# Performance work log

Measured on AMD Instinct MI355X. Metric: run time of the kernel, lower is better.

Reference implementation:

```python
import jax, jax.numpy as jnp
import numpy as np

ENC_DIMS = [768, 2048, 1024, 512, 128]   # [in_dim] + layers + [e_dim]
DEC_DIMS = ENC_DIMS[::-1]
NUM_LEVELS = 4    # len(num_emb_list)
NUM_EXPERTS = 10
CODEBOOK_K = 256  # codes per level per expert
BETA = 0.001


def setup_inputs() -> dict:
    key = jax.random.key(0)
    B = 32768
    ks = jax.random.split(key, 16)
    inp = {}
    inp["x"] = jax.random.normal(ks[0], (B, ENC_DIMS[0]), dtype=jnp.float32)
    inp["labels"] = jax.random.randint(ks[1], (B,), 0, NUM_EXPERTS)
    i = 2
    for l in range(4):
        inp[f"enc_w{l}"] = jax.random.normal(ks[i], (ENC_DIMS[l], ENC_DIMS[l + 1]), dtype=jnp.float32) * 0.02
        inp[f"enc_b{l}"] = jnp.zeros((ENC_DIMS[l + 1],), dtype=jnp.float32)
        i += 1
    for l in range(4):
        inp[f"dec_w{l}"] = jax.random.normal(ks[i], (DEC_DIMS[l], DEC_DIMS[l + 1]), dtype=jnp.float32) * 0.02
        inp[f"dec_b{l}"] = jnp.zeros((DEC_DIMS[l + 1],), dtype=jnp.float32)
        i += 1
    # per-level, per-expert codebooks: [L, E, K, D]
    inp["cb"] = jax.random.normal(ks[i], (NUM_LEVELS, NUM_EXPERTS, CODEBOOK_K, ENC_DIMS[-1]), dtype=jnp.float32) * 0.02
    return inp


def _mlp(h, ws, bs):
    # Linear + ReLU between layers, no activation on the last layer (dropout=0, bn=False)
    n = len(ws)
    for i in range(n):
        h = h @ ws[i] + bs[i]
        if i < n - 1:
            h = jax.nn.relu(h)
    return h


def _residual_quantize(z, labels, cb):
    # z: [B, D]; labels: [B] expert ids; cb: [L, E, K, D]
    res = z
    qsum = jnp.zeros_like(z)
    loss = jnp.zeros((), dtype=z.dtype)
    idx_list = []
    for l in range(cb.shape[0]):  # small fixed loop over quantization levels
        cbl = cb[l]  # [E, K, D]
        # squared distances to each sample's expert codebook:
        # d[b,k] = ||res_b||^2 - 2 res_b . C[lab_b,k] + ||C[lab_b,k]||^2
        dots = jnp.einsum('bd,ekd->bek', res, cbl)                       # [B, E, K]
        dots = jnp.take_along_axis(dots, labels[:, None, None], axis=1)[:, 0]  # [B, K]
        cnorm = jnp.sum(cbl * cbl, axis=-1)[labels]                      # [B, K]
        d = jnp.sum(res * res, axis=-1, keepdims=True) - 2.0 * dots + cnorm
        idx = jnp.argmin(d, axis=-1)                                     # [B]
        q = cbl[labels, idx]                                             # [B, D] gather
        # codebook loss + beta * commitment loss
        loss = loss + jnp.mean((q - jax.lax.stop_gradient(res)) ** 2) \
                    + BETA * jnp.mean((jax.lax.stop_gradient(q) - res) ** 2)
        qsum = qsum + q
        res = res - q
        idx_list.append(idx)
    # straight-through estimator on the full quantized vector
    x_q = z + jax.lax.stop_gradient(qsum - z)
    indices = jnp.stack(idx_list, axis=1)  # [B, L]
    return x_q, loss, indices


def reference(x, labels,
              enc_w0, enc_b0, enc_w1, enc_b1, enc_w2, enc_b2, enc_w3, enc_b3,
              dec_w0, dec_b0, dec_w1, dec_b1, dec_w2, dec_b2, dec_w3, dec_b3,
              cb):
    enc_ws = [enc_w0, enc_w1, enc_w2, enc_w3]
    enc_bs = [enc_b0, enc_b1, enc_b2, enc_b3]
    dec_ws = [dec_w0, dec_w1, dec_w2, dec_w3]
    dec_bs = [dec_b0, dec_b1, dec_b2, dec_b3]
    z = _mlp(x, enc_ws, enc_bs)                      # encoder -> [B, e_dim]
    x_q, rq_loss, indices = _residual_quantize(z, labels, cb)
    out = _mlp(x_q, dec_ws, dec_bs)                  # decoder -> [B, in_dim]
    return out, rq_loss, indices, x_q
```

## Files before the change

kernel.cpp:

```cpp
#include <hip/hip_runtime.h>
#include <cstdint>
#include <cstddef>


typedef _Float16 half8  __attribute__((ext_vector_type(8)));
typedef short    short8 __attribute__((ext_vector_type(8)));
typedef float    f32x4  __attribute__((ext_vector_type(4)));

__device__ __forceinline__ uint16_t f32_to_bf16(float v) {
    uint32_t u = __float_as_uint(v);
    u += 0x7fff + ((u >> 16) & 1);
    return (uint16_t)(u >> 16);
}
__device__ __forceinline__ uint16_t f32_to_f16_bits(float v) {
    _Float16 h = (_Float16)v;
    return __builtin_bit_cast(uint16_t, h);
}
__device__ __forceinline__ void split16(float v, uint16_t& hb, uint16_t& lb) {
    hb = f32_to_f16_bits(v);
    float hf = (float)__builtin_bit_cast(_Float16, hb);
    lb = f32_to_f16_bits((v - hf) * 2048.0f);
}

__device__ __forceinline__ float wave_sum(float v) {
    #pragma unroll
    for (int off = 32; off > 0; off >>= 1)
        v += __shfl_xor(v, off, 64);
    return v;
}

#define GLOAD_LDS16(g, l)                                                      \
    __builtin_amdgcn_global_load_lds(                                          \
        (const __attribute__((address_space(1))) void*)(g),                    \
        (__attribute__((address_space(3))) void*)(l), 16, 0, 0)

__device__ __forceinline__ void wait_vm(int nf) {
    if (nf >= 12)     asm volatile("s_waitcnt vmcnt(12)" ::: "memory");
    else if (nf >= 8) asm volatile("s_waitcnt vmcnt(8)"  ::: "memory");
    else if (nf >= 6) asm volatile("s_waitcnt vmcnt(6)"  ::: "memory");
    else if (nf >= 4) asm volatile("s_waitcnt vmcnt(4)"  ::: "memory");
    else              asm volatile("s_waitcnt vmcnt(0)"  ::: "memory");
}
__device__ __forceinline__ void wait_lg0() { asm volatile("s_waitcnt lgkmcnt(0)" ::: "memory"); }

template<bool F16> struct VecT        { using type = half8;  };
template<>         struct VecT<false> { using type = short8; };

__device__ __forceinline__ f32x4 mfma16(half8 a, half8 b, f32x4 c) {
    return __builtin_amdgcn_mfma_f32_16x16x32_f16(a, b, c, 0, 0, 0);
}
__device__ __forceinline__ f32x4 mfma16(short8 a, short8 b, f32x4 c) {
    return __builtin_amdgcn_mfma_f32_16x16x32_bf16(a, b, c, 0, 0, 0);
}

template<int NPL, int NBUF, int BN, bool ISF16, bool CORR, bool RELU, int OUT>
__global__ __launch_bounds__(256, 3)
void gemm_mfma(const uint16_t* __restrict__ A, const uint16_t* __restrict__ Wt,
               const float* __restrict__ bias,
               float* __restrict__ Cf, uint16_t* __restrict__ C0,
               uint16_t* __restrict__ C1, int M, int K, int N) {
    using vec8 = typename VecT<ISF16>::type;
    constexpr int APL    = 8192;
    constexpr int BPL    = BN * 64;
    constexpr int TILE_B = NPL * (APL + BPL);
    constexpr int BSHOT  = BN / 64;
    constexpr int NR     = BN / 32;
    constexpr int LPT    = NPL * (2 + BSHOT);
    __shared__ __align__(16) char lds[NBUF * TILE_B];

    const int t    = threadIdx.x;
    const int lane = t & 63, wave = t >> 6;
    const int wm = wave >> 1, wn = wave & 1;
    const int bm = blockIdx.y, bn = blockIdx.x;

    const size_t planeA = (size_t)M * K;
    const size_t planeB = (size_t)N * K;

    const int r0 = t >> 2,        c0 = (t & 3) ^ ((r0 >> 1) & 3);
    const int r1 = 64 + (t >> 2), c1 = (t & 3) ^ ((r1 >> 1) & 3);

    const uint16_t* gA0 = A + (size_t)(bm * 128 + r0) * K + c0 * 8;
    const uint16_t* gA1 = A + (size_t)(bm * 128 + r1) * K + c1 * 8;
    const uint16_t* gB[2];
    gB[0] = Wt + (size_t)(bn * BN + r0) * K + c0 * 8;
    if (BSHOT == 2) gB[1] = Wt + (size_t)(bn * BN + r1) * K + c1 * 8;

    const int wb = wave * 1024;
    const int l15 = lane & 15, quad = lane >> 4;
    const int cpf = quad ^ ((l15 >> 1) & 3);
    const int aoff = ((wm * 64 + l15) * 4 + cpf) * 16;
    const int boff = ((wn * (BN / 2) + l15) * 4 + cpf) * 16;

    f32x4 accM[4][NR], accC[4][NR];
    #pragma unroll
    for (int mi = 0; mi < 4; ++mi)
        #pragma unroll
        for (int nj = 0; nj < NR; ++nj)
            #pragma unroll
            for (int r = 0; r < 4; ++r) { accM[mi][nj][r] = 0.f; if (CORR) accC[mi][nj][r] = 0.f; }

    const int nt = K >> 5;

    auto stage = [&](int ti, int bi) {
        char* bA = (char*)lds + bi * TILE_B;
        char* bB = bA + NPL * APL;
        const int kb = ti * 32;
        #pragma unroll
        for (int p = 0; p < NPL; ++p) {
            GLOAD_LDS16(gA0 + (size_t)p * planeA + kb, bA + p * APL + wb);
            GLOAD_LDS16(gA1 + (size_t)p * planeA + kb, bA + p * APL + 4096 + wb);
            #pragma unroll
            for (int s = 0; s < BSHOT; ++s)
                GLOAD_LDS16(gB[s] + (size_t)p * planeB + kb, bB + p * BPL + s * 4096 + wb);
        }
    };

    #pragma unroll
    for (int i = 0; i < NBUF - 1; ++i) stage(i, i);

    int cur = 0;
    for (int it = 0; it < nt; ++it) {
        const int nx = it + NBUF - 1;
        if (nx < nt) {
            int bi = cur + NBUF - 1; if (bi >= NBUF) bi -= NBUF;
            stage(nx, bi);
        }
        const int rem = nt - 1 - it;
        const int nf  = (rem < NBUF - 1 ? rem : NBUF - 1) * LPT;
        wait_vm(nf);
        __builtin_amdgcn_sched_barrier(0);
        __builtin_amdgcn_s_barrier();
        __builtin_amdgcn_sched_barrier(0);

        char* bA = (char*)lds + cur * TILE_B;
        char* bB = bA + NPL * APL;

        vec8 a0[4], b0[NR];
        #pragma unroll
        for (int i = 0; i < 4; ++i)
            a0[i] = *(const vec8*)(bA + aoff + i * 1024);
        #pragma unroll
        for (int i = 0; i < NR; ++i)
            b0[i] = *(const vec8*)(bB + boff + i * 1024);
        #pragma unroll
        for (int mi = 0; mi < 4; ++mi)
            #pragma unroll
            for (int nj = 0; nj < NR; ++nj)
                accM[mi][nj] = mfma16(a0[mi], b0[nj], accM[mi][nj]);

        if (CORR) {
            vec8 b1[NR];
            #pragma unroll
            for (int i = 0; i < NR; ++i)
                b1[i] = *(const vec8*)(bB + BPL + boff + i * 1024);
            #pragma unroll
            for (int mi = 0; mi < 4; ++mi)
                #pragma unroll
                for (int nj = 0; nj < NR; ++nj)
                    accC[mi][nj] = mfma16(a0[mi], b1[nj], accC[mi][nj]);
            vec8 a1[4];
            #pragma unroll
            for (int i = 0; i < 4; ++i)
                a1[i] = *(const vec8*)(bA + APL + aoff + i * 1024);
            #pragma unroll
            for (int mi = 0; mi < 4; ++mi)
                #pragma unroll
                for (int nj = 0; nj < NR; ++nj)
                    accC[mi][nj] = mfma16(a1[mi], b0[nj], accC[mi][nj]);
        }

        wait_lg0();
        __builtin_amdgcn_sched_barrier(0);
        __builtin_amdgcn_s_barrier();
        __builtin_amdgcn_sched_barrier(0);

        cur = cur + 1; if (cur == NBUF) cur = 0;
    }

    if (CORR) {
        #pragma unroll
        for (int mi = 0; mi < 4; ++mi)
            #pragma unroll
            for (int nj = 0; nj < NR; ++nj)
                #pragma unroll
                for (int r = 0; r < 4; ++r)
                    accM[mi][nj][r] += accC[mi][nj][r] * (1.0f / 2048.0f);
    }

    const int colb = bn * BN + wn * (BN / 2) + l15;
    const int rowb = bm * 128 + wm * 64 + quad * 4;
    float bz[NR];
    #pragma unroll
    for (int nj = 0; nj < NR; ++nj) bz[nj] = bias[colb + nj * 16];

    #pragma unroll
    for (int mi = 0; mi < 4; ++mi)
        #pragma unroll
        for (int nj = 0; nj < NR; ++nj)
            #pragma unroll
            for (int r = 0; r < 4; ++r) {
                float v = accM[mi][nj][r] + bz[nj];
                if (RELU) v = fmaxf(v, 0.f);
                const size_t o = (size_t)(rowb + mi * 16 + r) * N + colb + nj * 16;
                if (OUT == 0) {
                    Cf[o] = v;
                } else if (OUT == 1) {
                    uint16_t hb, lb; split16(v, hb, lb);
                    C0[o] = hb; C1[o] = lb;
                } else {
                    C0[o] = f32_to_bf16(v);
                }
            }
}

template<int MODE>
__global__ __launch_bounds__(256)
void prep_w(const float* __restrict__ W, uint16_t* __restrict__ out, int K, int N) {
    __shared__ float tile[32][33];
    const int tx = threadIdx.x & 31, ty = threadIdx.x >> 5;
    const int n0 = blockIdx.x * 32, k0 = blockIdx.y * 32;
    #pragma unroll
    for (int i = 0; i < 4; ++i)
        tile[ty + i * 8][tx] = W[(size_t)(k0 + ty + i * 8) * N + n0 + tx];
    __syncthreads();
    #pragma unroll
    for (int i = 0; i < 4; ++i) {
        float v = tile[tx][ty + i * 8];
        size_t o = (size_t)(n0 + ty + i * 8) * K + k0 + tx;
        if (MODE == 0) {
            uint16_t hb, lb; split16(v, hb, lb);
            out[o] = hb;
            out[o + (size_t)N * K] = lb;
        } else {
            out[o] = f32_to_bf16(v);
        }
    }
}

__global__ __launch_bounds__(256)
void split_x(const float* __restrict__ x, uint16_t* __restrict__ hi,
             uint16_t* __restrict__ lo, int n4) {
    int i = blockIdx.x * 256 + threadIdx.x;
    const int stride = gridDim.x * 256;
    for (; i < n4; i += stride) {
        float4 v = ((const float4*)x)[i];
        ushort4 h, l;
        split16(v.x, h.x, l.x); split16(v.y, h.y, l.y);
        split16(v.z, h.z, l.z); split16(v.w, h.w, l.w);
        ((ushort4*)hi)[i] = h;
        ((ushort4*)lo)[i] = l;
    }
}

__global__ __launch_bounds__(256)
void prep_cb2(const float* __restrict__ cb, uint16_t* __restrict__ cbh,
              uint16_t* __restrict__ cbl, float* __restrict__ cnorm) {
    const int t = threadIdx.x, wave = t >> 6, lane = t & 63;
    const int row = blockIdx.x * 4 + wave;
    const float2 v = *(const float2*)(cb + (size_t)row * 128 + lane * 2);
    ushort2 h, l;
    split16(v.x, h.x, l.x); split16(v.y, h.y, l.y);
    *(ushort2*)(cbh + (size_t)row * 128 + lane * 2) = h;
    *(ushort2*)(cbl + (size_t)row * 128 + lane * 2) = l;
    const float s = wave_sum(v.x * v.x + v.y * v.y);
    if (lane == 0) cnorm[row] = s;
}

__global__ __launch_bounds__(256)
void hist_kernel(const int* __restrict__ labels, int* __restrict__ off,
                 int* __restrict__ cnt) {
    __shared__ int h[10];
    const int t = threadIdx.x;
    if (t < 10) h[t] = 0;
    __syncthreads();
    for (int i = t; i < 32768; i += 256) atomicAdd(&h[labels[i]], 1);
    __syncthreads();
    if (t == 0) {
        int a = 0;
        for (int e = 0; e < 10; ++e) { off[e] = a; a += h[e]; }
        off[10] = a;
    }
    if (t < 10) cnt[t] = 0;
}

__global__ __launch_bounds__(256)
void scatter_kernel(const int* __restrict__ labels, const int* __restrict__ off,
                    int* __restrict__ cnt, int* __restrict__ perm) {
    __shared__ int h[10], base[10];
    const int t = threadIdx.x;
    const int r = blockIdx.x * 256 + t;
    if (t < 10) h[t] = 0;
    __syncthreads();
    const int e = labels[r];
    const int lr = atomicAdd(&h[e], 1);
    __syncthreads();
    if (t < 10) base[t] = (h[t] > 0) ? atomicAdd(&cnt[t], h[t]) : 0;
    __syncthreads();
    perm[off[e] + base[e] + lr] = r;
}

__global__ __launch_bounds__(256)
void gather_kernel(const int* __restrict__ perm, const float* __restrict__ z,
                   float* __restrict__ resp, uint16_t* __restrict__ resph,
                   uint16_t* __restrict__ respl) {
    const int t = threadIdx.x, wave = t >> 6, lane = t & 63;
    const int p = blockIdx.x * 4 + wave;
    const int r = perm[p];
    const float2 v = *(const float2*)(z + (size_t)r * 128 + lane * 2);
    *(float2*)(resp + (size_t)p * 128 + lane * 2) = v;
    ushort2 h, l;
    split16(v.x, h.x, l.x); split16(v.y, h.y, l.y);
    *(ushort2*)(resph + (size_t)p * 128 + lane * 2) = h;
    *(ushort2*)(respl + (size_t)p * 128 + lane * 2) = l;
}

#define BETA_F 0.001f

template<bool LAST>
__global__ __launch_bounds__(256)
void rq_level(int l, const int* __restrict__ off, const int* __restrict__ perm,
              const float* __restrict__ cb, const uint16_t* __restrict__ cbh,
              const uint16_t* __restrict__ cbl, const float* __restrict__ cnorm,
              float* __restrict__ resp, uint16_t* __restrict__ resph,
              uint16_t* __restrict__ respl, const float* __restrict__ z,
              float* __restrict__ out_idx, float* __restrict__ out_xq,
              float* __restrict__ out_loss, uint16_t* __restrict__ xqbf) {
    __shared__ __align__(16) uint16_t Ah[2048], Al[2048];
    __shared__ __align__(16) uint16_t Bh[8192], Bl[8192];
    __shared__ float redv[64][4];
    __shared__ int   redk[64][4];
    __shared__ int   kwin[64];
    __shared__ float wl[4];
    __shared__ int   soff[11];

    const int t = threadIdx.x, lane = t & 63, wave = t >> 6;
    if (t < 11) soff[t] = off[t];
    __syncthreads();

    int e = -1, tile = 0, acc = 0;
    #pragma unroll
    for (int i = 0; i < 10; ++i) {
        const int nb = (soff[i + 1] - soff[i] + 63) >> 6;
        if ((int)blockIdx.x < acc + nb && e < 0) { e = i; tile = blockIdx.x - acc; }
        acc += nb;
    }
    if (e < 0) return;
    const int p0 = soff[e] + tile * 64;
    const int nrows = min(64, soff[e + 1] - p0);
    const int le = l * 10 + e;

    const int l15 = lane & 15, quad = lane >> 4;
    const int wn = wave;

    const int ar = t >> 2;
    const int ac = (t & 3) ^ ((ar >> 1) & 3);
    const int arp = p0 + ((ar < nrows) ? ar : 0);
    const uint16_t* gAh = resph + (size_t)arp * 128 + ac * 8;
    const uint16_t* gAl = respl + (size_t)arp * 128 + ac * 8;
    const uint16_t* cbh_b = cbh + (size_t)le * 256 * 128;
    const uint16_t* cbl_b = cbl + (size_t)le * 256 * 128;

    f32x4 accM[4][4], accC[4][4];
    #pragma unroll
    for (int mi = 0; mi < 4; ++mi)
        #pragma unroll
        for (int nj = 0; nj < 4; ++nj)
            #pragma unroll
            for (int r = 0; r < 4; ++r) { accM[mi][nj][r] = 0.f; accC[mi][nj][r] = 0.f; }

    const int cpf = quad ^ ((l15 >> 1) & 3);

    for (int kc = 0; kc < 4; ++kc) {
        const int kk = kc * 32;
        __syncthreads();
        GLOAD_LDS16(gAh + kk, (char*)Ah + t * 16);
        GLOAD_LDS16(gAl + kk, (char*)Al + t * 16);
        #pragma unroll
        for (int rnd = 0; rnd < 4; ++rnd) {
            const int j = rnd * 256 + t;
            const int br = j >> 2;
            const int bc = (j & 3) ^ ((br >> 1) & 3);
            GLOAD_LDS16(cbh_b + (size_t)br * 128 + kk + bc * 8, (char*)Bh + j * 16);
            GLOAD_LDS16(cbl_b + (size_t)br * 128 + kk + bc * 8, (char*)Bl + j * 16);
        }
        __syncthreads();

        half8 ah[4], bh[4];
        #pragma unroll
        for (int i = 0; i < 4; ++i) {
            ah[i] = *(const half8*)((char*)Ah + ((i * 16 + l15) * 4 + cpf) * 16);
            bh[i] = *(const half8*)((char*)Bh + ((wn * 64 + i * 16 + l15) * 4 + cpf) * 16);
        }
        #pragma unroll
        for (int mi = 0; mi < 4; ++mi)
            #pragma unroll
            for (int nj = 0; nj < 4; ++nj)
                accM[mi][nj] = mfma16(ah[mi], bh[nj], accM[mi][nj]);

        half8 bl4[4];
        #pragma unroll
        for (int i = 0; i < 4; ++i)
            bl4[i] = *(const half8*)((char*)Bl + ((wn * 64 + i * 16 + l15) * 4 + cpf) * 16);
        #pragma unroll
        for (int mi = 0; mi < 4; ++mi)
            #pragma unroll
            for (int nj = 0; nj < 4; ++nj)
                accC[mi][nj] = mfma16(ah[mi], bl4[nj], accC[mi][nj]);

        half8 al4[4];
        #pragma unroll
        for (int i = 0; i < 4; ++i)
            al4[i] = *(const half8*)((char*)Al + ((i * 16 + l15) * 4 + cpf) * 16);
        #pragma unroll
        for (int mi = 0; mi < 4; ++mi)
            #pragma unroll
            for (int nj = 0; nj < 4; ++nj)
                accC[mi][nj] = mfma16(al4[mi], bh[nj], accC[mi][nj]);
    }

    float cnv[4];
    #pragma unroll
    for (int nj = 0; nj < 4; ++nj)
        cnv[nj] = cnorm[le * 256 + wn * 64 + nj * 16 + l15];

    #pragma unroll
    for (int mi = 0; mi < 4; ++mi)
        #pragma unroll
        for (int r = 0; r < 4; ++r) {
            float bv = 1e30f; int bk = 0;
            #pragma unroll
            for (int nj = 0; nj < 4; ++nj) {
                const float d = cnv[nj] -
                    2.f * (accM[mi][nj][r] + accC[mi][nj][r] * (1.0f / 2048.0f));
                const int k = wn * 64 + nj * 16 + l15;
                if (d < bv || (d == bv && k < bk)) { bv = d; bk = k; }
            }
            #pragma unroll
            for (int o = 1; o < 16; o <<= 1) {
                const float ov = __shfl_xor(bv, o, 64);
                const int   ok = __shfl_xor(bk, o, 64);
                if (ov < bv || (ov == bv && ok < bk)) { bv = ov; bk = ok; }
            }
            const int row = mi * 16 + quad * 4 + r;
            if (l15 == 0) { redv[row][wn] = bv; redk[row][wn] = bk; }
        }
    __syncthreads();

    if (wave == 0) {
        const int row = lane;
        if (row < nrows) {
            float bv = redv[row][0]; int bk = redk[row][0];
            #pragma unroll
            for (int w = 1; w < 4; ++w) {
                const float ov = redv[row][w]; const int ok = redk[row][w];
                if (ov < bv || (ov == bv && ok < bk)) { bv = ov; bk = ok; }
            }
            kwin[row] = bk;
            out_idx[(size_t)perm[p0 + row] * 4 + l] = (float)bk;
        }
    }
    __syncthreads();

    float lossw = 0.f;
    for (int i = 0; i < 16; ++i) {
        const int row = wave * 16 + i;
        if (row < nrows) {
            const int p = p0 + row;
            const int k = kwin[row];
            const float2 q2 = *(const float2*)(cb + ((size_t)le * 256 + k) * 128 + lane * 2);
            float2 r2 = *(float2*)(resp + (size_t)p * 128 + lane * 2);
            const float n0 = r2.x - q2.x, n1 = r2.y - q2.y;
            *(float2*)(resp + (size_t)p * 128 + lane * 2) = make_float2(n0, n1);
            if (!LAST) {
                ushort2 h, lo;
                split16(n0, h.x, lo.x); split16(n1, h.y, lo.y);
                *(ushort2*)(resph + (size_t)p * 128 + lane * 2) = h;
                *(ushort2*)(respl + (size_t)p * 128 + lane * 2) = lo;
            }
            lossw += wave_sum(n0 * n0 + n1 * n1);
            if (LAST) {
                const int orig = perm[p];
                const float2 z2 = *(const float2*)(z + (size_t)orig * 128 + lane * 2);
                const float xq0 = z2.x - n0, xq1 = z2.y - n1;
                out_xq[(size_t)orig * 128 + lane * 2]     = xq0;
                out_xq[(size_t)orig * 128 + lane * 2 + 1] = xq1;
                ushort2 xb; xb.x = f32_to_bf16(xq0); xb.y = f32_to_bf16(xq1);
                *(ushort2*)(xqbf + (size_t)orig * 128 + lane * 2) = xb;
            }
        }
    }
    if (lane == 0) wl[wave] = lossw;
    __syncthreads();
    if (t == 0)
        atomicAdd(out_loss, (wl[0] + wl[1] + wl[2] + wl[3]) *
                            ((1.0f + BETA_F) / (32768.0f * 128.0f)));
}


extern "C" void kernel_launch(void* const* d_in, const int* in_sizes, int n_in,
                              void* d_out, int out_size, void* d_ws, size_t ws_size,
                              hipStream_t stream) {
    const float* x      = (const float*)d_in[0];
    const int*   labels = (const int*)d_in[1];
    const float* ew[4]  = {(const float*)d_in[2], (const float*)d_in[4],
                           (const float*)d_in[6], (const float*)d_in[8]};
    const float* eb[4]  = {(const float*)d_in[3], (const float*)d_in[5],
                           (const float*)d_in[7], (const float*)d_in[9]};
    const float* dw[4]  = {(const float*)d_in[10], (const float*)d_in[12],
                           (const float*)d_in[14], (const float*)d_in[16]};
    const float* db[4]  = {(const float*)d_in[11], (const float*)d_in[13],
                           (const float*)d_in[15], (const float*)d_in[17]};
    const float* cb     = (const float*)d_in[18];

    float* out = (float*)d_out;
    const size_t LOSS_OFF = 25165824;
    const size_t IDX_OFF  = 25165825;
    const size_t XQ_OFF   = 25296897;

    char* W = (char*)d_ws;
    size_t off_b = 0;
    auto alloc = [&](size_t bytes) { char* p = W + off_b; off_b += (bytes + 255) & ~(size_t)255; return p; };
    char*     region1 = alloc(134217728);
    char*     region2 = alloc(67108864);
    float*    z       = (float*)alloc(32768ull * 128 * 4);
    uint16_t* xqbf    = (uint16_t*)alloc(32768ull * 128 * 2);
    uint16_t* wtE0 = (uint16_t*)alloc(2ull *  768 * 2048 * 2);
    uint16_t* wtE1 = (uint16_t*)alloc(2ull * 2048 * 1024 * 2);
    uint16_t* wtE2 = (uint16_t*)alloc(2ull * 1024 *  512 * 2);
    uint16_t* wtE3 = (uint16_t*)alloc(2ull *  512 *  128 * 2);
    uint16_t* wtD0 = (uint16_t*)alloc(128ull  *  512 * 2);
    uint16_t* wtD1 = (uint16_t*)alloc(512ull  * 1024 * 2);
    uint16_t* wtD2 = (uint16_t*)alloc(1024ull * 2048 * 2);
    uint16_t* wtD3 = (uint16_t*)alloc(2048ull *  768 * 2);

    char* r1 = region1;
    float*    resp  = (float*)r1;                      r1 += 32768ull * 128 * 4;
    uint16_t* resph = (uint16_t*)r1;                   r1 += 32768ull * 128 * 2;
    uint16_t* respl = (uint16_t*)r1;                   r1 += 32768ull * 128 * 2;
    uint16_t* cbh   = (uint16_t*)r1;                   r1 += 4ull * 10 * 256 * 128 * 2;
    uint16_t* cbl   = (uint16_t*)r1;                   r1 += 4ull * 10 * 256 * 128 * 2;
    float*    cnorm = (float*)r1;                      r1 += 4ull * 10 * 256 * 4;
    int*      permv = (int*)r1;                        r1 += 32768ull * 4;
    int*      eoff  = (int*)r1;                        r1 += 16 * 4;
    int*      ecnt  = (int*)r1;                        r1 += 16 * 4;

    dim3 blk(256);

    prep_w<0><<<dim3(2048/32,  768/32), blk, 0, stream>>>(ew[0], wtE0,  768, 2048);
    prep_w<0><<<dim3(1024/32, 2048/32), blk, 0, stream>>>(ew[1], wtE1, 2048, 1024);
    prep_w<0><<<dim3( 512/32, 1024/32), blk, 0, stream>>>(ew[2], wtE2, 1024,  512);
    prep_w<0><<<dim3( 128/32,  512/32), blk, 0, stream>>>(ew[3], wtE3,  512,  128);
    prep_w<1><<<dim3( 512/32,  128/32), blk, 0, stream>>>(dw[0], wtD0,  128,  512);
    prep_w<1><<<dim3(1024/32,  512/32), blk, 0, stream>>>(dw[1], wtD1,  512, 1024);
    prep_w<1><<<dim3(2048/32, 1024/32), blk, 0, stream>>>(dw[2], wtD2, 1024, 2048);
    prep_w<1><<<dim3( 768/32, 2048/32), blk, 0, stream>>>(dw[3], wtD3, 2048,  768);

    const int MH = 16384;
    for (int half = 0; half < 2; ++half) {
        const float* xh = x + (size_t)half * MH * 768;
        uint16_t* xpl = (uint16_t*)region2;
        split_x<<<1024, blk, 0, stream>>>(xh, xpl, xpl + (size_t)MH * 768, MH * 768 / 4);

        uint16_t* h1 = (uint16_t*)region1;
        gemm_mfma<2, 2, 64, true, true, true, 1><<<dim3(32, 128), blk, 0, stream>>>(
            xpl, wtE0, eb[0], nullptr, h1, h1 + (size_t)MH * 2048, MH, 768, 2048);

        uint16_t* h2 = (uint16_t*)region2;
        gemm_mfma<2, 2, 64, true, true, true, 1><<<dim3(16, 128), blk, 0, stream>>>(
            h1, wtE1, eb[1], nullptr, h2, h2 + (size_t)MH * 1024, MH, 2048, 1024);

        uint16_t* h3 = (uint16_t*)region1;
        gemm_mfma<2, 2, 64, true, true, true, 1><<<dim3(8, 128), blk, 0, stream>>>(
            h2, wtE2, eb[2], nullptr, h3, h3 + (size_t)MH * 512, MH, 1024, 512);

        gemm_mfma<2, 2, 64, true, true, false, 0><<<dim3(2, 128), blk, 0, stream>>>(
            h3, wtE3, eb[3], z + (size_t)half * MH * 128, nullptr, nullptr, MH, 512, 128);
    }

    prep_cb2<<<2560, blk, 0, stream>>>(cb, cbh, cbl, cnorm);
    hist_kernel<<<1, blk, 0, stream>>>(labels, eoff, ecnt);
    scatter_kernel<<<128, blk, 0, stream>>>(labels, eoff, ecnt, permv);
    gather_kernel<<<8192, blk, 0, stream>>>(permv, z, resp, resph, respl);
    hipMemsetAsync((char*)d_out + LOSS_OFF * 4, 0, 4, stream);

    rq_level<false><<<522, blk, 0, stream>>>(0, eoff, permv, cb, cbh, cbl, cnorm,
        resp, resph, respl, z, out + IDX_OFF, out + XQ_OFF, out + LOSS_OFF, xqbf);
    rq_level<false><<<522, blk, 0, stream>>>(1, eoff, permv, cb, cbh, cbl, cnorm,
        resp, resph, respl, z, out + IDX_OFF, out + XQ_OFF, out + LOSS_OFF, xqbf);
    rq_level<false><<<522, blk, 0, stream>>>(2, eoff, permv, cb, cbh, cbl, cnorm,
        resp, resph, respl, z, out + IDX_OFF, out + XQ_OFF, out + LOSS_OFF, xqbf);
    rq_level<true ><<<522, blk, 0, stream>>>(3, eoff, permv, cb, cbh, cbl, cnorm,
        resp, resph, respl, z, out + IDX_OFF, out + XQ_OFF, out + LOSS_OFF, xqbf);

    const int M = 32768;
    uint16_t* d0 = (uint16_t*)region1;
    uint16_t* d1 = (uint16_t*)region2;
    uint16_t* d2 = (uint16_t*)region1;
    gemm_mfma<1, 3, 128, false, false, true, 2><<<dim3(4, 256), blk, 0, stream>>>(
        xqbf, wtD0, db[0], nullptr, d0, nullptr, M, 128, 512);
    gemm_mfma<1, 3, 128, false, false, true, 2><<<dim3(8, 256), blk, 0, stream>>>(
        d0, wtD1, db[1], nullptr, d1, nullptr, M, 512, 1024);
    gemm_mfma<1, 3, 128, false, false, true, 2><<<dim3(16, 256), blk, 0, stream>>>(
        d1, wtD2, db[2], nullptr, d2, nullptr, M, 1024, 2048);
    gemm_mfma<1, 3, 128, false, false, false, 0><<<dim3(6, 256), blk, 0, stream>>>(
        d2, wtD3, db[3], out, nullptr, nullptr, M, 2048, 768);
}
```

Before: 2.118 ms.

## Add 512-thread 128x256-tile MFMA GEMM with triple-buffered pipeline for large layers

Introduces a new GEMM kernel using 8 waves per block and a 128x256 output tile, with three LDS buffers and staged loads interleaved between the split-precision correction MFMA phases. It replaces the previous 64/128-wide-N kernels for the large encoder and decoder layers, and widens the last encoder layer's tile to 128. The larger tile raises arithmetic intensity and weight reuse per block, cutting global traffic and the number of blocks. The cost is higher register and LDS pressure, lower occupancy (2 blocks per CU), and dropping the occupancy hint on the old kernel.

```diff
diff --git a/kernel.cpp b/kernel.cpp
--- a/kernel.cpp
+++ b/kernel.cpp
@@ -41,6 +41,12 @@
     else if (nf >= 4) asm volatile("s_waitcnt vmcnt(4)"  ::: "memory");
     else              asm volatile("s_waitcnt vmcnt(0)"  ::: "memory");
 }
+template<int N>
+__device__ __forceinline__ void wait_vmK() {
+    if constexpr (N == 3)      asm volatile("s_waitcnt vmcnt(3)" ::: "memory");
+    else if constexpr (N == 6) asm volatile("s_waitcnt vmcnt(6)" ::: "memory");
+    else                       asm volatile("s_waitcnt vmcnt(0)" ::: "memory");
+}
 __device__ __forceinline__ void wait_lg0() { asm volatile("s_waitcnt lgkmcnt(0)" ::: "memory"); }
 
 template<bool F16> struct VecT        { using type = half8;  };
@@ -53,8 +59,182 @@
     return __builtin_amdgcn_mfma_f32_16x16x32_bf16(a, b, c, 0, 0, 0);
 }
 
+template<bool ISF16, bool CORR, bool RELU, int OUT>
+__global__ __launch_bounds__(512, 2)
+void gemm_256(const uint16_t* __restrict__ A, const uint16_t* __restrict__ Wt,
+              const float* __restrict__ bias,
+              float* __restrict__ Cf, uint16_t* __restrict__ C0,
+              uint16_t* __restrict__ C1, int M, int K, int N) {
+    using vec8 = typename VecT<ISF16>::type;
+    constexpr int NPL    = CORR ? 2 : 1;
+    constexpr int ABYT   = 8192;
+    constexpr int BBYT   = 16384;
+    constexpr int TILE_B = NPL * (ABYT + BBYT);
+    constexpr int NBUF   = 3;
+    constexpr int LPS    = CORR ? 6 : 3;
+    __shared__ __align__(16) char lds[NBUF * TILE_B];
+
+    const int t    = threadIdx.x;
+    const int lane = t & 63, wave = t >> 6;
+    const int wm = wave >> 2, wn = wave & 3;
+    const int bm = blockIdx.y, bn = blockIdx.x;
+
+    const size_t planeA = (size_t)M * K;
+    const size_t planeB = (size_t)N * K;
+
+    const int r = t >> 2;
+    const int c = (t & 3) ^ ((r >> 1) & 3);
+    const uint16_t* gA  = A  + (size_t)(bm * 128 + r) * K + c * 8;
+    const uint16_t* gB0 = Wt + (size_t)(bn * 256 + r) * K + c * 8;
+    const uint16_t* gB1 = Wt + (size_t)(bn * 256 + 128 + r) * K + c * 8;
+
+    const int l15 = lane & 15, quad = lane >> 4;
+    const int cpf = quad ^ ((l15 >> 1) & 3);
+    const int aoff = ((wm * 64 + l15) * 4 + cpf) * 16;
+    const int boff = ((wn * 64 + l15) * 4 + cpf) * 16;
+
+    f32x4 accM[4][4], accC[4][4];
+    #pragma unroll
+    for (int mi = 0; mi < 4; ++mi)
+        #pragma unroll
+        for (int nj = 0; nj < 4; ++nj)
+            #pragma unroll
+            for (int rr = 0; rr < 4; ++rr) { accM[mi][nj][rr] = 0.f; if (CORR) accC[mi][nj][rr] = 0.f; }
+
+    const int nt = K >> 5;
+
+    auto stageA = [&](int ti, int bi) {
+        char* b = (char*)lds + bi * TILE_B;
+        const int kb = ti * 32;
+        GLOAD_LDS16(gA + kb, b + t * 16);
+        if (CORR) GLOAD_LDS16(gA + planeA + kb, b + ABYT + t * 16);
+    };
+    auto stageBh = [&](int ti, int bi) {
+        char* b = (char*)lds + bi * TILE_B + NPL * ABYT;
+        const int kb = ti * 32;
+        GLOAD_LDS16(gB0 + kb, b + t * 16);
+        GLOAD_LDS16(gB1 + kb, b + 8192 + t * 16);
+    };
+    auto stageBl = [&](int ti, int bi) {
+        char* b = (char*)lds + bi * TILE_B + NPL * ABYT + BBYT;
+        const int kb = ti * 32;
+        GLOAD_LDS16(gB0 + planeB + kb, b + t * 16);
+        GLOAD_LDS16(gB1 + planeB + kb, b + 8192 + t * 16);
+    };
+
+    stageA(0, 0); stageBh(0, 0); if (CORR) stageBl(0, 0);
+    stageA(1, 1); stageBh(1, 1); if (CORR) stageBl(1, 1);
+    wait_vmK<LPS>();
+    __builtin_amdgcn_sched_barrier(0);
+    __builtin_amdgcn_s_barrier();
+    __builtin_amdgcn_sched_barrier(0);
+
+    int cur = 0;
+    for (int it = 0; it < nt; ++it) {
+        char* bufc = (char*)lds + cur * TILE_B;
+        const int nx = it + 2;
+        const bool st = nx < nt;
+        const int bi = (cur + 2 >= NBUF) ? cur + 2 - NBUF : cur + 2;
+
+        vec8 a0[4], b0[4];
+        #pragma unroll
+        for (int i = 0; i < 4; ++i) {
+            a0[i] = *(const vec8*)(bufc + aoff + i * 1024);
+            b0[i] = *(const vec8*)(bufc + NPL * ABYT + boff + i * 1024);
+        }
+        if (st) { stageA(nx, bi); if (!CORR) stageBh(nx, bi); }
+        __builtin_amdgcn_s_barrier();
+        wait_lg0();
+        __builtin_amdgcn_sched_barrier(0);
+        __builtin_amdgcn_s_setprio(1);
+        #pragma unroll
+        for (int mi = 0; mi < 4; ++mi)
+            #pragma unroll
+            for (int nj = 0; nj < 4; ++nj)
+                accM[mi][nj] = mfma16(a0[mi], b0[nj], accM[mi][nj]);
+        __builtin_amdgcn_s_setprio(0);
+
+        if (CORR) {
+            __builtin_amdgcn_s_barrier();
+            vec8 b1[4];
+            #pragma unroll
+            for (int i = 0; i < 4; ++i)
+                b1[i] = *(const vec8*)(bufc + NPL * ABYT + BBYT + boff + i * 1024);
+            if (st) stageBh(nx, bi);
+            __builtin_amdgcn_s_barrier();
+            wait_lg0();
+            __builtin_amdgcn_sched_barrier(0);
+            __builtin_amdgcn_s_setprio(1);
+            #pragma unroll
+            for (int mi = 0; mi < 4; ++mi)
+                #pragma unroll
+                for (int nj = 0; nj < 4; ++nj)
+                    accC[mi][nj] = mfma16(a0[mi], b1[nj], accC[mi][nj]);
+            __builtin_amdgcn_s_setprio(0);
+            __builtin_amdgcn_s_barrier();
+            vec8 a1[4];
+            #pragma unroll
+            for (int i = 0; i < 4; ++i)
+                a1[i] = *(const vec8*)(bufc + ABYT + aoff + i * 1024);
+            if (st) stageBl(nx, bi);
+            __builtin_amdgcn_s_barrier();
+            wait_lg0();
+            __builtin_amdgcn_sched_barrier(0);
+            __builtin_amdgcn_s_setprio(1);
+            #pragma unroll
+            for (int mi = 0; mi < 4; ++mi)
+                #pragma unroll
+                for (int nj = 0; nj < 4; ++nj)
+                    accC[mi][nj] = mfma16(a1[mi], b0[nj], accC[mi][nj]);
+            __builtin_amdgcn_s_setprio(0);
+        }
+
+        wait_vmK<LPS>();
+        __builtin_amdgcn_sched_barrier(0);
+        __builtin_amdgcn_s_barrier();
+        __builtin_amdgcn_sched_barrier(0);
+
+        cur = cur + 1; if (cur == NBUF) cur = 0;
+    }
+
+    if (CORR) {
+        #pragma unroll
+        for (int mi = 0; mi < 4; ++mi)
+            #pragma unroll
+            for (int nj = 0; nj < 4; ++nj)
+                #pragma unroll
+                for (int rr = 0; rr < 4; ++rr)
+                    accM[mi][nj][rr] += accC[mi][nj][rr] * (1.0f / 2048.0f);
+    }
+
+    const int colb = bn * 256 + wn * 64 + l15;
+    const int rowb = bm * 128 + wm * 64 + quad * 4;
+    float bz[4];
+    #pragma unroll
+    for (int nj = 0; nj < 4; ++nj) bz[nj] = bias[colb + nj * 16];
+
+    #pragma unroll
+    for (int mi = 0; mi < 4; ++mi)
+        #pragma unroll
+        for (int nj = 0; nj < 4; ++nj)
+            #pragma unroll
+            for (int rr = 0; rr < 4; ++rr) {
+                float v = accM[mi][nj][rr] + bz[nj];
+                if (RELU) v = fmaxf(v, 0.f);
+                const size_t o = (size_t)(rowb + mi * 16 + rr) * N + colb + nj * 16;
+                if (OUT == 0) {
+                    Cf[o] = v;
+                } else if (OUT == 1) {
+                    uint16_t hb, lb; split16(v, hb, lb);
+                    C0[o] = hb; C1[o] = lb;
+                } else {
+                    C0[o] = f32_to_bf16(v);
+                }
+            }
+}
+
 template<int NPL, int NBUF, int BN, bool ISF16, bool CORR, bool RELU, int OUT>
-__global__ __launch_bounds__(256, 3)
+__global__ __launch_bounds__(256)
 void gemm_mfma(const uint16_t* __restrict__ A, const uint16_t* __restrict__ Wt,
                const float* __restrict__ bias,
                float* __restrict__ Cf, uint16_t* __restrict__ C0,
@@ -545,6 +725,7 @@
     int*      ecnt  = (int*)r1;                        r1 += 16 * 4;
 
     dim3 blk(256);
+    dim3 blk512(512);
 
     prep_w<0><<<dim3(2048/32,  768/32), blk, 0, stream>>>(ew[0], wtE0,  768, 2048);
     prep_w<0><<<dim3(1024/32, 2048/32), blk, 0, stream>>>(ew[1], wtE1, 2048, 1024);
@@ -562,18 +743,18 @@
         split_x<<<1024, blk, 0, stream>>>(xh, xpl, xpl + (size_t)MH * 768, MH * 768 / 4);
 
         uint16_t* h1 = (uint16_t*)region1;
-        gemm_mfma<2, 2, 64, true, true, true, 1><<<dim3(32, 128), blk, 0, stream>>>(
+        gemm_256<true, true, true, 1><<<dim3(8, 128), blk512, 0, stream>>>(
             xpl, wtE0, eb[0], nullptr, h1, h1 + (size_t)MH * 2048, MH, 768, 2048);
 
         uint16_t* h2 = (uint16_t*)region2;
-        gemm_mfma<2, 2, 64, true, true, true, 1><<<dim3(16, 128), blk, 0, stream>>>(
+        gemm_256<true, true, true, 1><<<dim3(4, 128), blk512, 0, stream>>>(
             h1, wtE1, eb[1], nullptr, h2, h2 + (size_t)MH * 1024, MH, 2048, 1024);
 
         uint16_t* h3 = (uint16_t*)region1;
-        gemm_mfma<2, 2, 64, true, true, true, 1><<<dim3(8, 128), blk, 0, stream>>>(
+        gemm_256<true, true, true, 1><<<dim3(2, 128), blk512, 0, stream>>>(
             h2, wtE2, eb[2], nullptr, h3, h3 + (size_t)MH * 512, MH, 1024, 512);
 
-        gemm_mfma<2, 2, 64, true, true, false, 0><<<dim3(2, 128), blk, 0, stream>>>(
+        gemm_mfma<2, 2, 128, true, true, false, 0><<<dim3(1, 128), blk, 0, stream>>>(
             h3, wtE3, eb[3], z + (size_t)half * MH * 128, nullptr, nullptr, MH, 512, 128);
     }
 
@@ -598,10 +779,10 @@
     uint16_t* d2 = (uint16_t*)region1;
     gemm_mfma<1, 3, 128, false, false, true, 2><<<dim3(4, 256), blk, 0, stream>>>(
         xqbf, wtD0, db[0], nullptr, d0, nullptr, M, 128, 512);
-    gemm_mfma<1, 3, 128, false, false, true, 2><<<dim3(8, 256), blk, 0, stream>>>(
+    gemm_256<false, false, true, 2><<<dim3(4, 256), blk512, 0, stream>>>(
         d0, wtD1, db[1], nullptr, d1, nullptr, M, 512, 1024);
-    gemm_mfma<1, 3, 128, false, false, true, 2><<<dim3(16, 256), blk, 0, stream>>>(
+    gemm_256<false, false, true, 2><<<dim3(8, 256), blk512, 0, stream>>>(
         d1, wtD2, db[2], nullptr, d2, nullptr, M, 1024, 2048);
-    gemm_mfma<1, 3, 128, false, false, false, 0><<<dim3(6, 256), blk, 0, stream>>>(
+    gemm_256<false, false, false, 0><<<dim3(3, 256), blk512, 0, stream>>>(
         d2, wtD3, db[3], out, nullptr, nullptr, M, 2048, 768);
 }
```

Measured after the change: 1.815 ms. 14.3% less time.
